# Kernel optimization log

Measured on AMD Instinct MI355X. Metric: run time of the kernel, lower is better.

The kernel has to match this reference:

```python
import jax, jax.numpy as jnp
import numpy as np

SR = 44100
LOWEST_HZ = 55.0
N_FRAMES = 100
L_ORDER = 5                       # l_filter_order
NC = L_ORDER + 1                  # num_coefficients
NA = L_ORDER + 2                  # num_active_indexes
V = int(SR // LOWEST_HZ) + NA     # coeff_vector_size = 808
N_SAMPLES = 44100


def _nat_cubic_spline_eval(y, t_out):
    """Natural cubic spline through y (n_knots, d) on uniform knots in [0,1],
    evaluated at t_out (T,). Returns (T, d)."""
    n, d = y.shape
    h = 1.0 / (n - 1)
    # second derivatives M: natural BC -> M[0] = M[n-1] = 0, tridiagonal solve
    rhs = 6.0 * (y[2:] - 2.0 * y[1:-1] + y[:-2]) / h        # (n-2, d)
    T = (jnp.diag(jnp.full((n - 2,), 4.0 * h))
         + jnp.diag(jnp.full((n - 3,), h), 1)
         + jnp.diag(jnp.full((n - 3,), h), -1))
    M_in = jnp.linalg.solve(T, rhs)
    M = jnp.concatenate([jnp.zeros((1, d), y.dtype), M_in, jnp.zeros((1, d), y.dtype)])
    idx = jnp.clip((t_out / h).astype(jnp.int32), 0, n - 2)
    f = (t_out - idx.astype(y.dtype) * h)[:, None]          # fractional offset
    y0, y1 = y[idx], y[idx + 1]
    M0, M1 = M[idx], M[idx + 1]
    bcoef = (y1 - y0) / h - h * (2.0 * M0 + M1) / 6.0
    ccoef = 0.5 * M0
    dcoef = (M1 - M0) / (6.0 * h)
    return y0 + f * (bcoef + f * (ccoef + f * dcoef))


def _sample_wise_lpc(x, a):
    """Time-varying all-pole filter: y[t] = x[t] - sum_i a[t, i] * y[t-1-i].
    x: (T,), a: (T, p) -> y: (T,)."""
    p = a.shape[1]

    def step(hist, inp):
        xt, at = inp
        yt = xt - jnp.dot(at, hist)
        hist = jnp.concatenate([yt[None], hist[:-1]])
        return hist, yt

    _, y = jax.lax.scan(step, jnp.zeros((p,), x.dtype), (x, a))
    return y


def setup_inputs() -> dict:
    key = jax.random.key(0)
    k1, k2, k3, k4 = jax.random.split(key, 4)
    # delay in samples, ~[300, 500] -> f0 in [88, 147] Hz, safely inside V=808
    delay_len_frames = 300.0 + 200.0 * jax.random.uniform(k1, (N_FRAMES,), dtype=jnp.float32)
    raw_gain = jnp.full((1,), 2.5, jnp.float32)             # sigmoid -> ~0.924 loop gain
    # raw coeffs uniform in (-2, 0) like the torch init
    raw_coeff_frames = -2.0 * jax.random.uniform(k2, (N_FRAMES, NC), dtype=jnp.float32)
    excitation = jax.random.normal(k3, (N_SAMPLES,), dtype=jnp.float32)
    exc_coefficients = 0.01 * jax.random.normal(k4, (1, N_SAMPLES, 1), dtype=jnp.float32)
    return {"delay_len_frames": delay_len_frames, "raw_gain": raw_gain,
            "raw_coeff_frames": raw_coeff_frames, "excitation": excitation,
            "exc_coefficients": exc_coefficients, "n_samples": N_SAMPLES}


def reference(delay_len_frames, raw_gain, raw_coeff_frames, excitation,
              exc_coefficients, n_samples):
    # constrained, normalized loop-filter coefficients per frame
    gain = jax.nn.sigmoid(raw_gain)                          # (1,)
    sig = jax.nn.sigmoid(raw_coeff_frames)                   # (F, NC)
    b_frames = sig / jnp.sum(sig, -1, keepdims=True) * gain

    # upsample delay + coeffs jointly with one natural cubic spline
    params = jnp.concatenate([delay_len_frames[:, None], b_frames], axis=1)  # (F, NC+1)
    t_out = jnp.linspace(0.0, 1.0, n_samples)
    up = _nat_cubic_spline_eval(params, t_out)               # (T, NC+1)
    delay, b = up[:, 0], up[:, 1:]

    z = jnp.floor(delay).astype(jnp.int32)                   # integer delay
    alfa = delay - jnp.floor(delay)                          # fractional part

    # scatter-build the per-sample sparse filter rows into dense A (T, V)
    cols = z[:, None] + jnp.arange(NA)[None, :]              # (T, NA)
    first = (-(1.0 - alfa) * b[:, 0])[:, None]
    mid = -(alfa[:, None] * b[:, :-1] + (1.0 - alfa)[:, None] * b[:, 1:])
    last = (-alfa * b[:, -1])[:, None]
    vals = jnp.concatenate([first, mid, last], axis=1)       # (T, NA)
    A = jnp.zeros((n_samples, V), jnp.float32).at[
        jnp.arange(n_samples)[:, None], cols].set(vals)

    # excitation shaping (order-1 time-varying all-pole), then KS string loop
    x = _sample_wise_lpc(excitation, exc_coefficients[0])
    y = _sample_wise_lpc(x, A)
    return y
```

## Files before the change

kernel.cpp:

```cpp
#include <hip/hip_runtime.h>

#define NSMP 44100
#define NKNOT 100
#define NIV  (NKNOT - 1)
#define NCC 6
#define NAA 7
#define NTH 256
#define RING 1024
#define SEG ((NSMP + NTH - 1) / NTH)
#define GW 8

__device__ __forceinline__ float sigm(float x) { return 1.0f / (1.0f + expf(-x)); }

__device__ __forceinline__ void lean_barrier() {
    asm volatile("s_waitcnt lgkmcnt(0)" ::: "memory");
    __builtin_amdgcn_s_barrier();
}

__global__ __launch_bounds__(NTH, 1) void diffks_kernel(
    const float* __restrict__ dlf,
    const float* __restrict__ rg,
    const float* __restrict__ rcf,
    const float* __restrict__ exc,
    const float* __restrict__ ecoef,
    float* __restrict__ out)
{
    __shared__ float P[NKNOT][NAA];
    __shared__ float M[NKNOT][NAA];
    __shared__ float CP[NKNOT];
    __shared__ float4 CO[NIV][8];
    __shared__ float ring[RING];
    __shared__ float wp[4], wq[4];
    __shared__ int   s_minz;

    const int tid = threadIdx.x;
    const int lane = tid & 63;
    const int wav  = tid >> 6;
    const float H = 1.0f / 99.0f;
    const float INV = 1.0f / (float)(NSMP - 1);

    if (tid == 0) s_minz = 0x7fffffff;
    for (int i = tid; i < RING; i += NTH) ring[i] = 0.0f;

    if (tid < NKNOT) {
        float g = sigm(rg[0]);
        float s[NCC];
        float sum = 0.0f;
#pragma unroll
        for (int j = 0; j < NCC; ++j) { s[j] = sigm(rcf[tid * NCC + j]); sum += s[j]; }
        P[tid][0] = dlf[tid];
#pragma unroll
        for (int j = 0; j < NCC; ++j) P[tid][j + 1] = s[j] / sum * g;
    }
    __syncthreads();

    if (tid == 0) {
        float cp = 0.25f;
        CP[0] = cp;
        for (int i = 1; i < NKNOT - 2; ++i) {
            cp = H / (4.0f * H - H * CP[i - 1]);
            CP[i] = cp;
        }
    }
    __syncthreads();
    if (tid < NAA) {
        int c = tid;
        float rhs0  = 6.0f * (P[2][c] - 2.0f * P[1][c] + P[0][c]) / H;
        float dprev = rhs0 / (4.0f * H);
        M[1][c] = dprev;
        for (int i = 1; i < NKNOT - 2; ++i) {
            float rhs = 6.0f * (P[i + 2][c] - 2.0f * P[i + 1][c] + P[i][c]) / H;
            float m   = 4.0f * H - H * CP[i - 1];
            float d   = (rhs - H * dprev) / m;
            M[i + 1][c] = d;
            dprev = d;
        }
        float nxt = M[NKNOT - 2][c];
        for (int i = NKNOT - 4; i >= 0; --i) {
            float v = M[i + 1][c] - CP[i] * nxt;
            M[i + 1][c] = v;
            nxt = v;
        }
        M[0][c] = 0.0f;
        M[NKNOT - 1][c] = 0.0f;
    }
    __syncthreads();

    for (int iv = tid; iv < NIV; iv += NTH) {
#pragma unroll
        for (int c = 0; c < NAA; ++c) {
            float y0 = P[iv][c], y1 = P[iv + 1][c];
            float m0 = M[iv][c], m1 = M[iv + 1][c];
            float b  = (y1 - y0) * 99.0f - H * (2.0f * m0 + m1) * (1.0f / 6.0f);
            CO[iv][c] = make_float4(y0, b, 0.5f * m0, (m1 - m0) * (99.0f / 6.0f));
        }
    }
    __syncthreads();

    {
        int zl = 0x7fffffff;
        for (int t = tid; t < NSMP; t += NTH) {
            float tt = (float)t * INV;
            int idx = (int)(tt * 99.0f); if (idx > NIV - 1) idx = NIV - 1;
            float f = tt - (float)idx * H;
            float4 k = CO[idx][0];
            float d0 = k.x + f * (k.y + f * (k.z + f * k.w));
            zl = min(zl, (int)floorf(d0));
        }
        atomicMin(&s_minz, zl);
    }

    {
        int start = tid * SEG;
        int end   = min(start + SEG, NSMP);
        float p = 1.0f, q = 0.0f;
#pragma unroll 4
        for (int t = start; t < end; ++t) {
            float a = ecoef[t];
            q = fmaf(-a, q, exc[t]);
            p *= -a;
        }
#pragma unroll
        for (int d = 1; d < 64; d <<= 1) {
            float pp = __shfl_up(p, d);
            float qq = __shfl_up(q, d);
            if (lane >= d) { q = fmaf(p, qq, q); p *= pp; }
        }
        if (lane == 63) { wp[wav] = p; wq[wav] = q; }
        float pe = __shfl_up(p, 1);
        float qe = __shfl_up(q, 1);
        if (lane == 0) { pe = 1.0f; qe = 0.0f; }
        __syncthreads();
        float v = 0.0f;
        for (int w = 0; w < wav; ++w) v = fmaf(wp[w], v, wq[w]);
        float y = fmaf(pe, v, qe);
#pragma unroll 4
        for (int t = start; t < end; ++t) {
            y = fmaf(-ecoef[t], y, exc[t]);
            out[t] = y;
        }
    }
    __syncthreads();

    int C = min(NTH, s_minz + 1);
    if (C < 1) C = 1;

    for (int W0 = 0; W0 < NSMP; W0 += GW * C) {
        float vals[GW][NAA];
        float xs[GW], accs[GW];
        int bases[GW];

#pragma unroll
        for (int g = 0; g < GW; ++g) {
            int t = W0 + g * C + tid;
            bool act = (tid < C) && (t < NSMP);
            if (act) {
                float tt = (float)t * INV;
                int idx = (int)(tt * 99.0f); if (idx > NIV - 1) idx = NIV - 1;
                float f = tt - (float)idx * H;
                float r[NAA];
#pragma unroll
                for (int c = 0; c < NAA; ++c) {
                    float4 k = CO[idx][c];
                    r[c] = k.x + f * (k.y + f * (k.z + f * k.w));
                }
                float fl = floorf(r[0]);
                float alfa = r[0] - fl;
                float om = 1.0f - alfa;
                vals[g][0] = -om * r[1];
#pragma unroll
                for (int j = 1; j < NAA - 1; ++j) vals[g][j] = -(alfa * r[j] + om * r[j + 1]);
                vals[g][NAA - 1] = -alfa * r[NCC];
                bases[g] = t - 1 - (int)fl;
                xs[g] = out[t];
            }
        }

#pragma unroll
        for (int g = 0; g < GW; ++g) {
            int t = W0 + g * C + tid;
            bool act = (tid < C) && (t < NSMP);
            if (act) {
                int base = bases[g];
                float yv[NAA];
#pragma unroll
                for (int j = 0; j < NAA; ++j) {
                    int src = base - j;
                    yv[j] = (src >= 0) ? ring[src & (RING - 1)] : 0.0f;
                }
                float p0 = vals[g][0] * yv[0];
                float p1 = vals[g][1] * yv[1];
                float p2 = vals[g][2] * yv[2];
                float p3 = vals[g][3] * yv[3];
                float p4 = vals[g][4] * yv[4];
                float p5 = vals[g][5] * yv[5];
                float p6 = vals[g][6] * yv[6];
                float s = ((p0 + p1) + (p2 + p3)) + ((p4 + p5) + p6);
                float acc = xs[g] - s;
                ring[t & (RING - 1)] = acc;
                accs[g] = acc;
            }
            lean_barrier();
        }

#pragma unroll
        for (int g = 0; g < GW; ++g) {
            int t = W0 + g * C + tid;
            if ((tid < C) && (t < NSMP)) out[t] = accs[g];
        }
    }
}

extern "C" void kernel_launch(void* const* d_in, const int* in_sizes, int n_in,
                              void* d_out, int out_size, void* d_ws, size_t ws_size,
                              hipStream_t stream) {
    const float* dlf   = (const float*)d_in[0];
    const float* rg    = (const float*)d_in[1];
    const float* rcf   = (const float*)d_in[2];
    const float* exc   = (const float*)d_in[3];
    const float* ecoef = (const float*)d_in[4];
    float* out = (float*)d_out;
    hipLaunchKernelGGL(diffks_kernel, dim3(1), dim3(NTH), 0, stream,
                       dlf, rg, rcf, exc, ecoef, out);
}
```

Before: 149.4 us.

## Precompute per-sample filter records in workspace and prefetch them in the serial loop

Adds a fast kernel that computes each sample's seven filter taps, boundary masks, ring read address and excitation value in a parallel pre-pass and stores them in global workspace. The serial string loop then loads these records one window ahead, overlapping global-memory latency with the barrier-bound recurrence. It also mirrors the ring buffer so the seven reads use a contiguous address without wrap masking, and raises the block to 320 threads so more samples fit per window. The cost is an extra 1.6 MB of workspace traffic, a dependence on workspace being provided, and a fallback kernel kept for when it is not.

```diff
diff --git a/kernel.cpp b/kernel.cpp
--- a/kernel.cpp
+++ b/kernel.cpp
@@ -5,43 +5,30 @@
 #define NIV  (NKNOT - 1)
 #define NCC 6
 #define NAA 7
-#define NTH 256
 #define RING 1024
+#define GW 8
+
+#define NTH 320
 #define SEG ((NSMP + NTH - 1) / NTH)
-#define GW 8
+
+#define RADDR_OFF (NSMP * 32)
+#define WS_NEEDED ((size_t)NSMP * 32 + (size_t)NSMP * 4)
 
 __device__ __forceinline__ float sigm(float x) { return 1.0f / (1.0f + expf(-x)); }
 
 __device__ __forceinline__ void lean_barrier() {
     asm volatile("s_waitcnt lgkmcnt(0)" ::: "memory");
     __builtin_amdgcn_s_barrier();
-}
-
-__global__ __launch_bounds__(NTH, 1) void diffks_kernel(
-    const float* __restrict__ dlf,
-    const float* __restrict__ rg,
+    __builtin_amdgcn_sched_barrier(0);
+}
+
+
+__device__ __forceinline__ void prep_spline(
+    const float* __restrict__ dlf, const float* __restrict__ rg,
     const float* __restrict__ rcf,
-    const float* __restrict__ exc,
-    const float* __restrict__ ecoef,
-    float* __restrict__ out)
+    float (*P)[NAA], float (*M)[NAA], float* CP, float4 (*CO)[8], int tid)
 {
-    __shared__ float P[NKNOT][NAA];
-    __shared__ float M[NKNOT][NAA];
-    __shared__ float CP[NKNOT];
-    __shared__ float4 CO[NIV][8];
-    __shared__ float ring[RING];
-    __shared__ float wp[4], wq[4];
-    __shared__ int   s_minz;
-
-    const int tid = threadIdx.x;
-    const int lane = tid & 63;
-    const int wav  = tid >> 6;
     const float H = 1.0f / 99.0f;
-    const float INV = 1.0f / (float)(NSMP - 1);
-
-    if (tid == 0) s_minz = 0x7fffffff;
-    for (int i = tid; i < RING; i += NTH) ring[i] = 0.0f;
-
     if (tid < NKNOT) {
         float g = sigm(rg[0]);
         float s[NCC];
@@ -53,7 +40,6 @@
         for (int j = 0; j < NCC; ++j) P[tid][j + 1] = s[j] / sum * g;
     }
     __syncthreads();
-
     if (tid == 0) {
         float cp = 0.25f;
         CP[0] = cp;
@@ -85,8 +71,7 @@
         M[NKNOT - 1][c] = 0.0f;
     }
     __syncthreads();
-
-    for (int iv = tid; iv < NIV; iv += NTH) {
+    for (int iv = tid; iv < NIV; iv += blockDim.x) {
 #pragma unroll
         for (int c = 0; c < NAA; ++c) {
             float y0 = P[iv][c], y1 = P[iv + 1][c];
@@ -96,16 +81,80 @@
         }
     }
     __syncthreads();
+}
+
+
+__global__ __launch_bounds__(NTH, 1) void diffks_fast(
+    const float* __restrict__ dlf, const float* __restrict__ rg,
+    const float* __restrict__ rcf, const float* __restrict__ exc,
+    const float* __restrict__ ecoef, float* __restrict__ out,
+    float4* __restrict__ rec, int* __restrict__ raddr)
+{
+    __shared__ float  P[NKNOT][NAA];
+    __shared__ float  M[NKNOT][NAA];
+    __shared__ float  CP[NKNOT];
+    __shared__ float4 CO[NIV][8];
+    __shared__ float  ring[2 * RING];
+    __shared__ float  wp[NTH / 64], wq[NTH / 64];
+    __shared__ int    s_minz;
+
+    const int tid  = threadIdx.x;
+    const int lane = tid & 63;
+    const int wav  = tid >> 6;
+    const float H   = 1.0f / 99.0f;
+    const float INV = 1.0f / (float)(NSMP - 1);
+
+    if (tid == 0) s_minz = 0x7fffffff;
+    for (int i = tid; i < 2 * RING; i += NTH) ring[i] = 0.0f;
+
+    prep_spline(dlf, rg, rcf, P, M, CP, CO, tid);
 
     {
+        int start = tid * SEG;
+        int end   = min(start + SEG, NSMP);
         int zl = 0x7fffffff;
-        for (int t = tid; t < NSMP; t += NTH) {
+        int cidx = -1;
+        float4 k0, k1, k2, k3, k4, k5, k6;
+        k0 = k1 = k2 = k3 = k4 = k5 = k6 = make_float4(0.f, 0.f, 0.f, 0.f);
+        for (int t = start; t < end; ++t) {
             float tt = (float)t * INV;
             int idx = (int)(tt * 99.0f); if (idx > NIV - 1) idx = NIV - 1;
+            if (idx != cidx) {
+                k0 = CO[idx][0]; k1 = CO[idx][1]; k2 = CO[idx][2]; k3 = CO[idx][3];
+                k4 = CO[idx][4]; k5 = CO[idx][5]; k6 = CO[idx][6];
+                cidx = idx;
+            }
             float f = tt - (float)idx * H;
-            float4 k = CO[idx][0];
-            float d0 = k.x + f * (k.y + f * (k.z + f * k.w));
-            zl = min(zl, (int)floorf(d0));
+            float r0 = k0.x + f * (k0.y + f * (k0.z + f * k0.w));
+            float r1 = k1.x + f * (k1.y + f * (k1.z + f * k1.w));
+            float r2 = k2.x + f * (k2.y + f * (k2.z + f * k2.w));
+            float r3 = k3.x + f * (k3.y + f * (k3.z + f * k3.w));
+            float r4 = k4.x + f * (k4.y + f * (k4.z + f * k4.w));
+            float r5 = k5.x + f * (k5.y + f * (k5.z + f * k5.w));
+            float r6 = k6.x + f * (k6.y + f * (k6.z + f * k6.w));
+            float fl = floorf(r0);
+            int z = (int)fl;
+            float alfa = r0 - fl, om = 1.0f - alfa;
+            float v0 = -om * r1;
+            float v1 = -(alfa * r1 + om * r2);
+            float v2 = -(alfa * r2 + om * r3);
+            float v3 = -(alfa * r3 + om * r4);
+            float v4 = -(alfa * r4 + om * r5);
+            float v5 = -(alfa * r5 + om * r6);
+            float v6 = -alfa * r6;
+            int base = t - 1 - z;
+            float w0 = (base - 6 >= 0) ? v6 : 0.0f;
+            float w1 = (base - 5 >= 0) ? v5 : 0.0f;
+            float w2 = (base - 4 >= 0) ? v4 : 0.0f;
+            float w3 = (base - 3 >= 0) ? v3 : 0.0f;
+            float w4 = (base - 2 >= 0) ? v2 : 0.0f;
+            float w5 = (base - 1 >= 0) ? v1 : 0.0f;
+            float w6 = (base     >= 0) ? v0 : 0.0f;
+            rec[2 * t] = make_float4(w0, w1, w2, w3);
+            float* rb = (float*)&rec[2 * t + 1];
+            rb[0] = w4; rb[1] = w5; rb[2] = w6;
+            raddr[t] = (base - 6) & (RING - 1);
+            zl = min(zl, z);
         }
         atomicMin(&s_minz, zl);
     }
@@ -134,7 +183,127 @@
         float v = 0.0f;
         for (int w = 0; w < wav; ++w) v = fmaf(wp[w], v, wq[w]);
         float y = fmaf(pe, v, qe);
+        float* recf = (float*)rec;
 #pragma unroll 4
+        for (int t = start; t < end; ++t) {
+            y = fmaf(-ecoef[t], y, exc[t]);
+            recf[8 * t + 7] = y;
+        }
+    }
+    __syncthreads();
+
+    int C = s_minz + 1;
+    if (C > NTH) C = NTH;
+    if (C < 1) C = 1;
+    const int step = GW * C;
+
+    float4 qa[GW], qb[GW];
+    int ra[GW];
+#pragma unroll
+    for (int g = 0; g < GW; ++g) {
+        int t = g * C + tid;
+        bool lv = (tid < C) && (t < NSMP);
+        if (lv) { qa[g] = rec[2 * t]; qb[g] = rec[2 * t + 1]; ra[g] = raddr[t]; }
+        else    { qa[g] = make_float4(0.f,0.f,0.f,0.f); qb[g] = qa[g]; ra[g] = 0; }
+    }
+
+    for (int W0 = 0; W0 < NSMP; W0 += step) {
+        const int Wn = W0 + step;
+        float4 na[GW], nb[GW];
+        int nr[GW];
+#pragma unroll
+        for (int g = 0; g < GW; ++g) {
+            int t = Wn + g * C + tid;
+            bool lv = (tid < C) && (t < NSMP);
+            if (lv) { na[g] = rec[2 * t]; nb[g] = rec[2 * t + 1]; nr[g] = raddr[t]; }
+            else    { na[g] = make_float4(0.f,0.f,0.f,0.f); nb[g] = na[g]; nr[g] = 0; }
+        }
+#pragma unroll
+        for (int g = 0; g < GW; ++g) {
+            int t = W0 + g * C + tid;
+            bool act = (tid < C) && (t < NSMP);
+            if (act) {
+                const float* rp = &ring[(unsigned)ra[g]];
+                float y0 = rp[0], y1 = rp[1], y2 = rp[2], y3 = rp[3];
+                float y4 = rp[4], y5 = rp[5], y6 = rp[6];
+                float s = ((qa[g].x * y0 + qa[g].y * y1) + (qa[g].z * y2 + qa[g].w * y3))
+                        + ((qb[g].x * y4 + qb[g].y * y5) + qb[g].z * y6);
+                float acc = qb[g].w - s;
+                int wi = t & (RING - 1);
+                ring[wi] = acc;
+                ring[wi + RING] = acc;
+                out[t] = acc;
+            }
+            lean_barrier();
+        }
+#pragma unroll
+        for (int g = 0; g < GW; ++g) { qa[g] = na[g]; qb[g] = nb[g]; ra[g] = nr[g]; }
+    }
+}
+
+
+#define FNTH 256
+#define FSEG ((NSMP + FNTH - 1) / FNTH)
+
+__global__ __launch_bounds__(FNTH, 1) void diffks_fallback(
+    const float* __restrict__ dlf, const float* __restrict__ rg,
+    const float* __restrict__ rcf, const float* __restrict__ exc,
+    const float* __restrict__ ecoef, float* __restrict__ out)
+{
+    __shared__ float  P[NKNOT][NAA];
+    __shared__ float  M[NKNOT][NAA];
+    __shared__ float  CP[NKNOT];
+    __shared__ float4 CO[NIV][8];
+    __shared__ float  ring[RING];
+    __shared__ float  wp[4], wq[4];
+    __shared__ int    s_minz;
+
+    const int tid = threadIdx.x;
+    const int lane = tid & 63;
+    const int wav  = tid >> 6;
+    const float H   = 1.0f / 99.0f;
+    const float INV = 1.0f / (float)(NSMP - 1);
+
+    if (tid == 0) s_minz = 0x7fffffff;
+    for (int i = tid; i < RING; i += FNTH) ring[i] = 0.0f;
+
+    prep_spline(dlf, rg, rcf, P, M, CP, CO, tid);
+
+    {
+        int zl = 0x7fffffff;
+        for (int t = tid; t < NSMP; t += FNTH) {
+            float tt = (float)t * INV;
+            int idx = (int)(tt * 99.0f); if (idx > NIV - 1) idx = NIV - 1;
+            float f = tt - (float)idx * H;
+            float4 k = CO[idx][0];
+            float d0 = k.x + f * (k.y + f * (k.z + f * k.w));
+            zl = min(zl, (int)floorf(d0));
+        }
+        atomicMin(&s_minz, zl);
+    }
+    {
+        int start = tid * FSEG;
+        int end   = min(start + FSEG, NSMP);
+        float p = 1.0f, q = 0.0f;
+        for (int t = start; t < end; ++t) {
+            float a = ecoef[t];
+            q = fmaf(-a, q, exc[t]);
+            p *= -a;
+        }
+#pragma unroll
+        for (int d = 1; d < 64; d <<= 1) {
+            float pp = __shfl_up(p, d);
+            float qq = __shfl_up(q, d);
+            if (lane >= d) { q = fmaf(p, qq, q); p *= pp; }
+        }
+        if (lane == 63) { wp[wav] = p; wq[wav] = q; }
+        float pe = __shfl_up(p, 1);
+        float qe = __shfl_up(q, 1);
+        if (lane == 0) { pe = 1.0f; qe = 0.0f; }
+        __syncthreads();
+        float v = 0.0f;
+        for (int w = 0; w < wav; ++w) v = fmaf(wp[w], v, wq[w]);
+        float y = fmaf(pe, v, qe);
         for (int t = start; t < end; ++t) {
             y = fmaf(-ecoef[t], y, exc[t]);
             out[t] = y;
@@ -142,14 +311,13 @@
     }
     __syncthreads();
 
-    int C = min(NTH, s_minz + 1);
+    int C = min(FNTH, s_minz + 1);
     if (C < 1) C = 1;
 
     for (int W0 = 0; W0 < NSMP; W0 += GW * C) {
         float vals[GW][NAA];
         float xs[GW], accs[GW];
         int bases[GW];
-
 #pragma unroll
         for (int g = 0; g < GW; ++g) {
             int t = W0 + g * C + tid;
@@ -175,7 +343,6 @@
                 xs[g] = out[t];
             }
         }
-
 #pragma unroll
         for (int g = 0; g < GW; ++g) {
             int t = W0 + g * C + tid;
@@ -202,7 +369,6 @@
             }
             lean_barrier();
         }
-
 #pragma unroll
         for (int g = 0; g < GW; ++g) {
             int t = W0 + g * C + tid;
@@ -220,6 +386,14 @@
     const float* exc   = (const float*)d_in[3];
     const float* ecoef = (const float*)d_in[4];
     float* out = (float*)d_out;
-    hipLaunchKernelGGL(diffks_kernel, dim3(1), dim3(NTH), 0, stream,
-                       dlf, rg, rcf, exc, ecoef, out);
-}
+
+    if (ws_size >= WS_NEEDED && d_ws != nullptr) {
+        float4* rec  = (float4*)d_ws;
+        int* raddr_p = (int*)((char*)d_ws + RADDR_OFF);
+        hipLaunchKernelGGL(diffks_fast, dim3(1), dim3(NTH), 0, stream,
+                           dlf, rg, rcf, exc, ecoef, out, rec, raddr_p);
+    } else {
+        hipLaunchKernelGGL(diffks_fallback, dim3(1), dim3(FNTH), 0, stream,
+                           dlf, rg, rcf, exc, ecoef, out);
+    }
+}
```

New measurement: 193.4 us. 29.5% more time.
